# Kernel tuning notes

Hardware: AMD Instinct MI355X
Metric: run time of the kernel (lower is better)

Reference implementation:

```python
import jax, jax.numpy as jnp
import numpy as np

B, N, E, D, L, NC = 48, 96, 1024, 300, 4, 7
NEG = 1e30


def _gru(x, h, w_ih, w_hh, b_ih, b_hh):
    # torch.nn.GRUCell math; weights are (3D, D) in torch layout
    gi = x @ w_ih.T + b_ih
    gh = h @ w_hh.T + b_hh
    ir, iz, inn = jnp.split(gi, 3, axis=-1)
    hr, hz, hn = jnp.split(gh, 3, axis=-1)
    r = jax.nn.sigmoid(ir + hr)
    z = jax.nn.sigmoid(iz + hz)
    n = jnp.tanh(inn + r * hn)
    return (1.0 - z) * n + z * h


def _layer(Cin, Hin, adj, cwi, cwh, cbi, cbh, pwi, pwh, pbi, pbh, wq, wk, gb):
    b, n, d = Cin.shape
    zeros = jnp.zeros((b, d), Cin.dtype)
    c0 = _gru(Cin[:, 0], zeros, cwi, cwh, cbi, cbh)          # GRUCell with h=0
    p0 = _gru(zeros, Cin[:, 0], pwi, pwh, pbi, pbh)          # M=0 at step 0
    P0 = jnp.zeros_like(Cin).at[:, 0].set(p0)                # growing P kept as full buffer
    pos = jnp.arange(n)

    def step(P, i):
        q = Cin[:, i]                                        # (B, D)
        mask = adj[:, i] * (pos < i).astype(adj.dtype)       # only predecessors j < i
        # GatLinear: Linear(cat(Q,K)) == Q.wq + K.wk + b
        alpha = (q @ wq)[:, None] + P @ wk + gb              # (B, N)
        alpha = alpha - (1.0 - mask) * NEG                   # mask_logic
        w = jax.nn.softmax(alpha, axis=-1)
        M = jnp.einsum('bn,bnd->bd', w, P)
        c_i = _gru(q, M, cwi, cwh, cbi, cbh)
        p_i = _gru(M, Hin[:, i], pwi, pwh, pbi, pbh)
        P = jax.lax.dynamic_update_slice(P, p_i[:, None, :], (0, i, 0))
        return P, c_i

    P, Cs = jax.lax.scan(step, P0, jnp.arange(1, n))
    CL = jnp.concatenate([c0[:, None], jnp.moveaxis(Cs, 0, 1)], axis=1)  # (B, N, D)
    return CL, P


def reference(features, adj, s_mask, fc1_w, fc1_b,
              gc_wih, gc_whh, gc_bih, gc_bhh,
              gp_wih, gp_whh, gp_bih, gp_bhh,
              gat_wq, gat_wk, gat_b,
              mlp_w0, mlp_b0, mlp_w1, mlp_b1, mlp_w2, mlp_b2):
    # s_mask is unused when no_rel_attn=True (faithful to torch forward)
    H0 = jax.nn.relu(features @ fc1_w + fc1_b)
    H_list = [H0]
    C_list = [H0]
    for l in range(L):
        CL, P = _layer(C_list[l], H_list[l], adj,
                       gc_wih[l], gc_whh[l], gc_bih[l], gc_bhh[l],
                       gp_wih[l], gp_whh[l], gp_bih[l], gp_bhh[l],
                       gat_wq[l], gat_wk[l], gat_b[l])
        C_list.append(CL)
        H_list.append(CL)
        H_list.append(P)
    H_list.append(features)
    H = jnp.concatenate(H_list, axis=2)                      # (B, N, 9D + E)
    x = jax.nn.relu(H @ mlp_w0 + mlp_b0)
    x = jax.nn.relu(x @ mlp_w1 + mlp_b1)
    logits = x @ mlp_w2 + mlp_b2                             # (B, N, NC)
    return logits


def setup_inputs() -> dict:
    key = jax.random.key(0)
    ks = jax.random.split(key, 25)
    s = 0.02

    def p(k, shape):
        return jax.random.normal(k, shape, jnp.float32) * s

    features = jax.random.normal(ks[0], (B, N, E), jnp.float32)
    # DAG adjacency: random predecessors, strictly lower-triangular, previous
    # utterance always connected (guarantees a nonempty attention context)
    base = jax.random.bernoulli(ks[1], 0.5, (B, N, N)).astype(jnp.float32)
    tri = jnp.tril(jnp.ones((N, N), jnp.float32), -1)
    prev = jnp.eye(N, k=-1, dtype=jnp.float32)
    adj = jnp.maximum(base * tri, prev[None])
    s_mask = jax.random.randint(ks[2], (B, N, N), 0, 2, jnp.int32)
    in_dim = D * (2 * L + 1) + E
    return {
        'features': features, 'adj': adj, 's_mask': s_mask,
        'fc1_w': p(ks[3], (E, D)), 'fc1_b': p(ks[4], (D,)),
        'gc_wih': p(ks[5], (L, 3 * D, D)), 'gc_whh': p(ks[6], (L, 3 * D, D)),
        'gc_bih': p(ks[7], (L, 3 * D)), 'gc_bhh': p(ks[8], (L, 3 * D)),
        'gp_wih': p(ks[9], (L, 3 * D, D)), 'gp_whh': p(ks[10], (L, 3 * D, D)),
        'gp_bih': p(ks[11], (L, 3 * D)), 'gp_bhh': p(ks[12], (L, 3 * D)),
        'gat_wq': p(ks[13], (L, D)), 'gat_wk': p(ks[14], (L, D)), 'gat_b': p(ks[15], (L,)),
        'mlp_w0': p(ks[16], (in_dim, D)), 'mlp_b0': p(ks[17], (D,)),
        'mlp_w1': p(ks[18], (D, D)), 'mlp_b1': p(ks[19], (D,)),
        'mlp_w2': p(ks[20], (D, NC)), 'mlp_b2': p(ks[21], (NC,)),
    }
```

## Files before the change

### kernel.cpp

```cpp
#include <hip/hip_runtime.h>
#include <math.h>

#define BB 48
#define NN 96
#define EE 1024
#define DD 300
#define LL 4
#define G3 900
#define PP 150
#define PP2 152
#define NC4 38
#define HDIM 3724
#define ROWS (BB*NN)
#define NEGI -1.0e30f
#define KP300 304
#define GIC_TILES 540

#define NLDS 6
#define NPIN 14

typedef _Float16 half2_t __attribute__((ext_vector_type(2)));
typedef _Float16 h8 __attribute__((ext_vector_type(8)));
typedef float f4 __attribute__((ext_vector_type(4)));

__device__ __forceinline__ float sigm(float x){
    return __fdividef(1.0f, 1.0f + __expf(-x));
}
__device__ __forceinline__ float ftanh(float x){
    float e = __expf(2.0f*x);
    return 1.0f - __fdividef(2.0f, e + 1.0f);
}

__device__ __forceinline__ void dot4(const h8 wv, const h8 mc,
                                     float& a0, float& a1, float& a2, float& a3)
{
    half2_t w0,w1,w2,w3,m0,m1,m2,m3;
    w0.x=wv[0]; w0.y=wv[1]; m0.x=mc[0]; m0.y=mc[1];
    w1.x=wv[2]; w1.y=wv[3]; m1.x=mc[2]; m1.y=mc[3];
    w2.x=wv[4]; w2.y=wv[5]; m2.x=mc[4]; m2.y=mc[5];
    w3.x=wv[6]; w3.y=wv[7]; m3.x=mc[6]; m3.y=mc[7];
    a0 = __builtin_amdgcn_fdot2(w0, m0, a0, false);
    a1 = __builtin_amdgcn_fdot2(w1, m1, a1, false);
    a2 = __builtin_amdgcn_fdot2(w2, m2, a2, false);
    a3 = __builtin_amdgcn_fdot2(w3, m3, a3, false);
}

__global__ __launch_bounds__(256) void pack_w_q(const float* __restrict__ src_all,
                                                h8* __restrict__ dst)
{
    int l = blockIdx.y;
    int idx = blockIdx.x*256 + threadIdx.x;
    if (idx >= NC4*G3) return;
    int c = idx / G3, gate = idx % G3;
    const float* src = src_all + (size_t)l*G3*DD + (size_t)gate*DD;
    h8 v;
    #pragma unroll
    for (int j=0;j<8;j++){
        int d = 8*c + j;
        v[j] = (d<DD) ? (_Float16)src[d] : (_Float16)0.f;
    }
    dst[(size_t)l*NC4*G3 + idx] = v;
}

__global__ __launch_bounds__(256) void conv_gru_w(const float* __restrict__ gp_whh,
                                                  const float* __restrict__ gc_wih,
                                                  const float* __restrict__ gc_whh,
                                                  _Float16* __restrict__ outp)
{
    int z = blockIdx.y; int l = z/3, wsel = z%3;
    const float* src = (wsel==0?gp_whh:wsel==1?gc_wih:gc_whh) + (size_t)l*G3*DD;
    _Float16* dst = outp + (size_t)z*G3*KP300;
    int idx = blockIdx.x*256 + threadIdx.x;
    if (idx >= G3*KP300) return;
    int n = idx/KP300, k = idx%KP300;
    dst[idx] = (k<DD) ? (_Float16)src[(size_t)n*DD+k] : (_Float16)0.f;
}

__global__ __launch_bounds__(256) void convT(const float* __restrict__ src,
                                             _Float16* __restrict__ dst,
                                             int K, int N, int Kpad)
{
    int idx = blockIdx.x*256 + threadIdx.x;
    if (idx >= N*Kpad) return;
    int n = idx/Kpad, k = idx%Kpad;
    dst[idx] = (k<K) ? (_Float16)src[(size_t)k*N + n] : (_Float16)0.f;
}

__device__ __forceinline__ void gemm_tile(
    int m0, int n0, int tid,
    const float* __restrict__ A, int lda,
    const _Float16* __restrict__ B, int Kpad,
    const float* __restrict__ bias,
    float* __restrict__ C, int ldc,
    int N, int K, int relu,
    _Float16 (*As)[40], _Float16 (*Bs)[40])
{
    int w = tid>>6, lane = tid&63;
    int wy = w>>1, wx = w&1;
    int lm = lane&15, q = lane>>4;

    f4 acc[4][2];
    #pragma unroll
    for (int a=0;a<4;a++)
        #pragma unroll
        for (int b=0;b<2;b++)
            #pragma unroll
            for (int r=0;r<4;r++) acc[a][b][r]=0.f;

    int am = tid>>1, akg = (tid&1)*16;
    int bn = tid>>2, bkg = (tid&3)*8;
    const float* arow = A + (size_t)(m0+am)*lda;

    for (int k0=0; k0<K; k0+=32){
        {
            __align__(16) _Float16 av[16];
            #pragma unroll
            for (int u=0;u<16;u+=4){
                int k = k0 + akg + u;
                float x0,x1,x2,x3;
                if (k+4 <= K){
                    float4 v = *(const float4*)(arow + k);
                    x0=v.x;x1=v.y;x2=v.z;x3=v.w;
                } else {
                    x0 = (k  <K)? arow[k  ]:0.f;
                    x1 = (k+1<K)? arow[k+1]:0.f;
                    x2 = (k+2<K)? arow[k+2]:0.f;
                    x3 = (k+3<K)? arow[k+3]:0.f;
                }
                av[u]=(_Float16)x0; av[u+1]=(_Float16)x1;
                av[u+2]=(_Float16)x2; av[u+3]=(_Float16)x3;
            }
            *(h8*)&As[am][akg]   = *(h8*)&av[0];
            *(h8*)&As[am][akg+8] = *(h8*)&av[8];
        }
        {
            int gk = k0 + bkg;
            h8 bv;
            #pragma unroll
            for (int j=0;j<8;j++) bv[j]=(_Float16)0.f;
            if (n0+bn < N && gk < Kpad)
                bv = *(const h8*)(B + (size_t)(n0+bn)*Kpad + gk);
            *(h8*)&Bs[bn][bkg] = bv;
        }
        __syncthreads();
        h8 af[4], bf[2];
        #pragma unroll
        for (int mb=0; mb<4; mb++) af[mb] = *(h8*)&As[wy*64+mb*16+lm][q*8];
        #pragma unroll
        for (int nb=0; nb<2; nb++) bf[nb] = *(h8*)&Bs[wx*32+nb*16+lm][q*8];
        #pragma unroll
        for (int mb=0; mb<4; mb++)
            #pragma unroll
            for (int nb=0; nb<2; nb++)
                acc[mb][nb] = __builtin_amdgcn_mfma_f32_16x16x32_f16(af[mb], bf[nb], acc[mb][nb], 0,0,0);
        __syncthreads();
    }
    #pragma unroll
    for (int mb=0; mb<4; mb++){
        int r0 = m0 + wy*64 + mb*16 + q*4;
        #pragma unroll
        for (int nb=0; nb<2; nb++){
            int c = n0 + wx*32 + nb*16 + lm;
            if (c < N){
                float bb = bias[c];
                #pragma unroll
                for (int reg=0; reg<4; reg++){
                    float v = acc[mb][nb][reg] + bb;
                    if (relu) v = fmaxf(v, 0.f);
                    C[(size_t)(r0+reg)*ldc + c] = v;
                }
            }
        }
    }
}

__global__ __launch_bounds__(256) void gemm_mfma(
    const float* __restrict__ A, int lda,
    const _Float16* __restrict__ B, int Kpad,
    const float* __restrict__ bias,
    float* __restrict__ C, int ldc,
    int N, int K, int relu)
{
    __shared__ _Float16 As[128][40];
    __shared__ _Float16 Bs[64][40];
    gemm_tile(blockIdx.y*128, blockIdx.x*64, threadIdx.x,
              A, lda, B, Kpad, bias, C, ldc, N, K, relu, As, Bs);
}

__global__ void featcopy(const float* __restrict__ f, float* __restrict__ H)
{
    size_t row = blockIdx.x;
    int t = threadIdx.x;
    float4 v = *(const float4*)(f + row*EE + t*4);
    *(float4*)(H + row*HDIM + 2700 + t*4) = v;
}

__global__ void __launch_bounds__(1024)
__attribute__((amdgpu_waves_per_eu(4,4)))
scan_kernel(
    float* __restrict__ Hbuf,
    const float* __restrict__ GHp,
    const h8* __restrict__ pwiQ,
    const h8* __restrict__ pwhQ,
    const float* __restrict__ pbi,
    const float* __restrict__ pbh,
    const float* __restrict__ wk,
    const float* __restrict__ wq,
    const float* __restrict__ gat_b, int lidx,
    const float* __restrict__ adj,
    float* __restrict__ Mbuf,
    int ccol, int hcol, int pcol,
    const _Float16* __restrict__ cwiF,
    const float* __restrict__ cbi,
    float* __restrict__ GIc)
{
    __shared__ __align__(16) char pool[158976];
    (void)wq; (void)gat_b; (void)lidx;

    if (blockIdx.x >= BB){
        if (threadIdx.x < 256){
            _Float16 (*As)[40] = (_Float16 (*)[40])pool;
            _Float16 (*Bs)[40] = (_Float16 (*)[40])(pool + 128*40*2);
            int bid = blockIdx.x - BB;
            int n0 = (bid % 15)*64, m0 = (bid / 15)*128;
            gemm_tile(m0, n0, threadIdx.x, Hbuf + ccol, HDIM, cwiF, KP300,
                      cbi, GIc, G3, G3, DD, 0, As, Bs);
        }
        return;
    }

    int b = blockIdx.x;
    int t = threadIdx.x;

    half2_t (*P_h2)[PP]   = (half2_t (*)[PP])(pool);
    h8*      Wlds         = (h8*)(pool + 57600);
    float*   g_s          = (float*)(pool + 144000);
    float  (*Mpart)[DD]   = (float (*)[DD])(pool + 147600);
    float*   ghp_s        = (float*)(pool + 151200);
    float*   hv_s         = (float*)(pool + 154800);
    half2_t* M_h2         = (half2_t*)(pool + 156000);
    float*   e_s          = (float*)(pool + 156640);
    float*   pk_s         = (float*)(pool + 157024);
    float*   pksum        = (float*)(pool + 157408);
    unsigned (*adjb)[4]   = (unsigned (*)[4])(pool + 157440);

    size_t rowbase = (size_t)b*NN;

    float pbi_r = (t < G3) ? pbi[t] : 0.f;
    float2 wk_r = make_float2(0.f,0.f);
    if (t < PP) wk_r = *(const float2*)&wk[2*t];

    h8 wp0,wp1,wp2,wp3,wp4,wp5,wp6,wp7,wp8,wp9,wp10,wp11,wp12,wp13;
    if (t < G3){
        const h8* W = pwiQ + t;
        wp0 = W[(size_t)6*G3];   wp1 = W[(size_t)7*G3];   wp2 = W[(size_t)8*G3];
        wp3 = W[(size_t)9*G3];   wp4 = W[(size_t)10*G3];  wp5 = W[(size_t)11*G3];
        wp6 = W[(size_t)12*G3];  wp7 = W[(size_t)13*G3];  wp8 = W[(size_t)14*G3];
        wp9 = W[(size_t)15*G3];  wp10 = W[(size_t)16*G3]; wp11 = W[(size_t)17*G3];
        wp12 = W[(size_t)18*G3]; wp13 = W[(size_t)19*G3];
        asm volatile("" : "+v"(wp0),"+v"(wp1),"+v"(wp2),"+v"(wp3),
                          "+v"(wp4),"+v"(wp5),"+v"(wp6));
        asm volatile("" : "+v"(wp7),"+v"(wp8),"+v"(wp9),"+v"(wp10),
                          "+v"(wp11),"+v"(wp12),"+v"(wp13));
    }

    for (int idx=t; idx<NLDS*G3; idx+=1024)
        Wlds[idx] = pwiQ[idx];
    if (t < NN*3){
        int r = t/3, w = t%3;
        const float* arow = adj + (rowbase + r)*NN + w*32;
        unsigned m = 0;
        for (int c=0;c<32;c++) if (arow[c] != 0.f) m |= (1u<<c);
        adjb[r][w] = m;
    }
    if (t < PP){
        float2 c2 = *(const float2*)&Hbuf[rowbase*HDIM + ccol + 2*t];
        Mpart[0][2*t] = c2.x; Mpart[0][2*t+1] = c2.y;
        half2_t mh; mh.x = (_Float16)c2.x; mh.y = (_Float16)c2.y;
        M_h2[t] = mh;
    } else if (t < PP2){
        half2_t z; z.x=(_Float16)0.f; z.y=(_Float16)0.f;
        M_h2[t] = z;
    }
    __syncthreads();
    if (t < G3){
        const h8* W2 = pwhQ + t;
        float a0=0.f, a1=0.f, a2=0.f, a3=0.f;
        #pragma unroll 4
        for (int c=0;c<NC4;c++){
            h8 wv = W2[(size_t)c*G3];
            h8 mc = *(h8*)&M_h2[4*c];
            dot4(wv, mc, a0,a1,a2,a3);
        }
        g_s[t] = pbh[t] + (a0+a2) + (a1+a3);
    }
    __syncthreads();
    if (t < 192){
        float pw = 0.f;
        if (t < PP){
            int d0 = 2*t, d1 = 2*t+1;
            float r0  = sigm(pbi[d0]      + g_s[d0]);
            float z0  = sigm(pbi[DD+d0]   + g_s[DD+d0]);
            float n0  = ftanh(pbi[2*DD+d0] + r0*g_s[2*DD+d0]);
            float p0  = (1.f-z0)*n0 + z0*Mpart[0][d0];
            float r1  = sigm(pbi[d1]      + g_s[d1]);
            float z1  = sigm(pbi[DD+d1]   + g_s[DD+d1]);
            float n1  = ftanh(pbi[2*DD+d1] + r1*g_s[2*DD+d1]);
            float p1  = (1.f-z1)*n1 + z1*Mpart[0][d1];
            *(float2*)&Hbuf[rowbase*HDIM + pcol + d0] = make_float2(p0,p1);
            half2_t ph; ph.x = (_Float16)p0; ph.y = (_Float16)p1;
            P_h2[0][t] = ph;
            pw = p0*wk_r.x + p1*wk_r.y;
            *(float2*)&Mbuf[rowbase*DD + d0] = make_float2(0.f,0.f);
        }
        #pragma unroll
        for (int o=32;o>0;o>>=1) pw += __shfl_xor(pw,o);
        if ((t&63)==0) pksum[t>>6] = pw;
    }
    __syncthreads();

    float m_run = NEGI;

    for (int i=1;i<NN;i++){
        size_t row = rowbase + i;
        if (t < 64){
            float s_last = pksum[0]+pksum[1]+pksum[2];
            if (t==0) pk_s[i-1] = s_last;
            m_run = fmaxf(m_run, s_last);
            float a0 = NEGI, a1 = NEGI;
            if (t < i){
                if ((adjb[i][t>>5]>>(t&31))&1u) a0 = (t==i-1)? s_last : pk_s[t];
            }
            int j1 = 64+t;
            if (t < 32 && j1 < i){
                if ((adjb[i][2]>>t)&1u) a1 = (j1==i-1)? s_last : pk_s[j1];
            }
            float e0 = __expf(a0 - m_run);
            float e1 = (t<32)? __expf(a1 - m_run) : 0.f;
            float ss = e0+e1;
            #pragma unroll
            for (int o=32;o>0;o>>=1) ss += __shfl_xor(ss,o);
            float inv = __fdividef(1.f, ss);
            e_s[t] = e0*inv;
            if (t<32) e_s[64+t] = e1*inv;
        }
        __syncthreads();
        if (t < 450){
            int g = t/150, dp = t%150;
            int cnt = (i+2)/3;
            int j0 = g*cnt; int j1 = j0+cnt; if (j1 > i) j1 = i;
            float m0=0.f, m1=0.f;
            #pragma unroll 4
            for (int j=j0;j<j1;j++){
                float w = e_s[j];
                half2_t pv = P_h2[j][dp];
                m0 += w*(float)pv.x;
                m1 += w*(float)pv.y;
            }
            *(float2*)&Mpart[g][2*dp] = make_float2(m0,m1);
        } else if (t >= 512){
            int k = t-512;
            #pragma unroll
            for (int it=0; it<2; it++){
                int idx = k + it*512;
                if (idx < 450){
                    *(float2*)&ghp_s[2*idx] = *(const float2*)&GHp[row*G3 + 2*idx];
                } else if (idx < 600){
                    int h = idx-450;
                    *(float2*)&hv_s[2*h] = *(const float2*)&Hbuf[row*HDIM + hcol + 2*h];
                }
            }
        }
        __syncthreads();
        if (t < PP){
            float m0 = Mpart[0][2*t] + Mpart[1][2*t] + Mpart[2][2*t];
            float m1 = Mpart[0][2*t+1] + Mpart[1][2*t+1] + Mpart[2][2*t+1];
            half2_t mh; mh.x = (_Float16)m0; mh.y = (_Float16)m1;
            M_h2[t] = mh;
            *(float2*)&Mbuf[row*DD + 2*t] = make_float2(m0,m1);
        }
        __syncthreads();
        if (t < G3){
            const h8* W = pwiQ + t;
            const h8* Mc = (const h8*)M_h2;
            float a0=0.f, a1=0.f, a2=0.f, a3=0.f;
            dot4(Wlds[t],        Mc[0], a0,a1,a2,a3);
            dot4(Wlds[G3+t],     Mc[1], a0,a1,a2,a3);
            dot4(Wlds[2*G3+t],   Mc[2], a0,a1,a2,a3);
            dot4(Wlds[3*G3+t],   Mc[3], a0,a1,a2,a3);
            dot4(Wlds[4*G3+t],   Mc[4], a0,a1,a2,a3);
            dot4(Wlds[5*G3+t],   Mc[5], a0,a1,a2,a3);
            dot4(wp0,  Mc[6],  a0,a1,a2,a3);
            dot4(wp1,  Mc[7],  a0,a1,a2,a3);
            dot4(wp2,  Mc[8],  a0,a1,a2,a3);
            dot4(wp3,  Mc[9],  a0,a1,a2,a3);
            dot4(wp4,  Mc[10], a0,a1,a2,a3);
            dot4(wp5,  Mc[11], a0,a1,a2,a3);
            dot4(wp6,  Mc[12], a0,a1,a2,a3);
            dot4(wp7,  Mc[13], a0,a1,a2,a3);
            dot4(wp8,  Mc[14], a0,a1,a2,a3);
            dot4(wp9,  Mc[15], a0,a1,a2,a3);
            dot4(wp10, Mc[16], a0,a1,a2,a3);
            dot4(wp11, Mc[17], a0,a1,a2,a3);
            dot4(wp12, Mc[18], a0,a1,a2,a3);
            dot4(wp13, Mc[19], a0,a1,a2,a3);
            #pragma unroll 6
            for (int c=NLDS+NPIN;c<NC4;c++){
                h8 wv = W[(size_t)c*G3];
                dot4(wv, Mc[c], a0,a1,a2,a3);
            }
            g_s[t] = pbi_r + (a0+a2) + (a1+a3);
        }
        __syncthreads();
        if (t < 192){
            float pw = 0.f;
            if (t < PP){
                int d0 = 2*t, d1 = 2*t+1;
                float2 hv = *(const float2*)&hv_s[d0];
                float r0  = sigm(g_s[d0]      + ghp_s[d0]);
                float z0  = sigm(g_s[DD+d0]   + ghp_s[DD+d0]);
                float n0  = ftanh(g_s[2*DD+d0] + r0*ghp_s[2*DD+d0]);
                float p0  = (1.f-z0)*n0 + z0*hv.x;
                float r1  = sigm(g_s[d1]      + ghp_s[d1]);
                float z1  = sigm(g_s[DD+d1]   + ghp_s[DD+d1]);
                float n1  = ftanh(g_s[2*DD+d1] + r1*ghp_s[2*DD+d1]);
                float p1  = (1.f-z1)*n1 + z1*hv.y;
                *(float2*)&Hbuf[row*HDIM + pcol + d0] = make_float2(p0,p1);
                half2_t ph; ph.x = (_Float16)p0; ph.y = (_Float16)p1;
                P_h2[i][t] = ph;
                pw = p0*wk_r.x + p1*wk_r.y;
            }
            #pragma unroll
            for (int o=32;o>0;o>>=1) pw += __shfl_xor(pw,o);
            if ((t&63)==0) pksum[t>>6] = pw;
        }
        __syncthreads();
    }
}

__global__ __launch_bounds__(320) void combine_c(
    const float* __restrict__ GIc, const float* __restrict__ GHc,
    const float* __restrict__ Mbuf, float* __restrict__ Hbuf, int clcol)
{
    size_t row = blockIdx.x;
    int d = threadIdx.x;
    if (d < DD){
        float ir = GIc[row*G3+d], iz = GIc[row*G3+DD+d], inn = GIc[row*G3+2*DD+d];
        float hr = GHc[row*G3+d], hz = GHc[row*G3+DD+d], hn  = GHc[row*G3+2*DD+d];
        float r  = sigm(ir+hr);
        float z  = sigm(iz+hz);
        float nn = ftanh(inn + r*hn);
        float h  = Mbuf[row*DD+d];
        Hbuf[row*HDIM + clcol + d] = (1.f-z)*nn + z*h;
    }
}

__global__ __launch_bounds__(64) void logits_kernel(
    const float* __restrict__ x2, const float* __restrict__ w2,
    const float* __restrict__ b2, float* __restrict__ out)
{
    size_t row = blockIdx.x;
    int lane = threadIdx.x;
    float acc[7]={0,0,0,0,0,0,0};
    for (int d=lane; d<DD; d+=64){
        float x = x2[row*DD+d];
        #pragma unroll
        for (int c=0;c<7;c++) acc[c] += x*w2[d*7+c];
    }
    #pragma unroll
    for (int c=0;c<7;c++){
        float s = acc[c];
        #pragma unroll
        for (int o=32;o>0;o>>=1) s += __shfl_down(s,o);
        if (lane==0) out[row*7+c] = s + b2[c];
    }
}

extern "C" void kernel_launch(void* const* d_in, const int* in_sizes, int n_in,
                              void* d_out, int out_size, void* d_ws, size_t ws_size,
                              hipStream_t stream)
{
    const float* features = (const float*)d_in[0];
    const float* adj      = (const float*)d_in[1];
    const float* fc1_w    = (const float*)d_in[3];
    const float* fc1_b    = (const float*)d_in[4];
    const float* gc_wih   = (const float*)d_in[5];
    const float* gc_whh   = (const float*)d_in[6];
    const float* gc_bih   = (const float*)d_in[7];
    const float* gc_bhh   = (const float*)d_in[8];
    const float* gp_wih   = (const float*)d_in[9];
    const float* gp_whh   = (const float*)d_in[10];
    const float* gp_bih   = (const float*)d_in[11];
    const float* gp_bhh   = (const float*)d_in[12];
    const float* gat_wq   = (const float*)d_in[13];
    const float* gat_wk   = (const float*)d_in[14];
    const float* gat_b    = (const float*)d_in[15];
    const float* mlp_w0   = (const float*)d_in[16];
    const float* mlp_b0   = (const float*)d_in[17];
    const float* mlp_w1   = (const float*)d_in[18];
    const float* mlp_b1   = (const float*)d_in[19];
    const float* mlp_w2   = (const float*)d_in[20];
    const float* mlp_b2   = (const float*)d_in[21];
    float* out = (float*)d_out;

    float* ws = (float*)d_ws;
    size_t off = 0;
    float* Hbuf = ws + off; off += (size_t)ROWS*HDIM;
    float* bufA = ws + off; off += (size_t)ROWS*G3;
    float* bufB = ws + off; off += (size_t)ROWS*G3;
    float* bufC = ws + off; off += (size_t)ROWS*G3;
    float* Mbuf = ws + off; off += (size_t)ROWS*DD;
    h8* pwiQ = (h8*)(ws + off); off += (size_t)LL*NC4*G3*4;
    h8* pwhQ = (h8*)(ws + off); off += (size_t)LL*NC4*G3*4;
    _Float16* gruF = (_Float16*)(ws + off); off += (size_t)12*G3*KP300/2;
    _Float16* fc1F = (_Float16*)(ws + off); off += (size_t)DD*EE/2;
    _Float16* mlp0F= (_Float16*)(ws + off); off += (size_t)DD*3728/2;
    _Float16* mlp1F= (_Float16*)(ws + off); off += (size_t)DD*KP300/2;
    (void)ws_size; (void)in_sizes; (void)n_in; (void)out_size;

    {
        pack_w_q<<<dim3((NC4*G3+255)/256, LL), 256, 0, stream>>>(gp_wih, pwiQ);
        pack_w_q<<<dim3((NC4*G3+255)/256, LL), 256, 0, stream>>>(gp_whh, pwhQ);
        conv_gru_w<<<dim3((G3*KP300+255)/256, 12), 256, 0, stream>>>(gp_whh, gc_wih, gc_whh, gruF);
        convT<<<(DD*EE+255)/256, 256, 0, stream>>>(fc1_w, fc1F, EE, DD, EE);
        convT<<<(DD*3728+255)/256, 256, 0, stream>>>(mlp_w0, mlp0F, HDIM, DD, 3728);
        convT<<<(DD*KP300+255)/256, 256, 0, stream>>>(mlp_w1, mlp1F, DD, DD, KP300);
    }
    gemm_mfma<<<dim3(5,36),256,0,stream>>>(features, EE, fc1F, EE, fc1_b,
                                           Hbuf, HDIM, DD, EE, 1);
    featcopy<<<ROWS,256,0,stream>>>(features, Hbuf);

    for (int l=0;l<LL;l++){
        int ccol  = (l==0)? 0 : 300 + (l-1)*600;
        int hcol  = l*300;
        int pcol  = 600 + l*600;
        int clcol = 300 + l*600;
        const h8* pwiQl = pwiQ + (size_t)l*NC4*G3;
        const h8* pwhQl = pwhQ + (size_t)l*NC4*G3;
        const _Float16* pwhF = gruF + (size_t)(l*3+0)*G3*KP300;
        const _Float16* cwiF = gruF + (size_t)(l*3+1)*G3*KP300;
        const _Float16* cwhF = gruF + (size_t)(l*3+2)*G3*KP300;

        gemm_mfma<<<dim3(15,36),256,0,stream>>>(Hbuf+hcol, HDIM, pwhF, KP300,
                                                gp_bhh + l*G3, bufA, G3, G3, DD, 0);
        scan_kernel<<<BB+GIC_TILES,1024,0,stream>>>(Hbuf, bufA, pwiQl, pwhQl,
                                          gp_bih + l*G3, gp_bhh + l*G3,
                                          gat_wk + l*DD, gat_wq + l*DD, gat_b, l,
                                          adj, Mbuf, ccol, hcol, pcol,
                                          cwiF, gc_bih + l*G3, bufB);
        gemm_mfma<<<dim3(15,36),256,0,stream>>>(Mbuf, DD, cwhF, KP300,
                                                gc_bhh + l*G3, bufC, G3, G3, DD, 0);
        combine_c<<<ROWS,320,0,stream>>>(bufB, bufC, Mbuf, Hbuf, clcol);
    }

    gemm_mfma<<<dim3(5,36),256,0,stream>>>(Hbuf, HDIM, mlp0F, 3728, mlp_b0,
                                           bufB, DD, DD, HDIM, 1);
    gemm_mfma<<<dim3(5,36),256,0,stream>>>(bufB, DD, mlp1F, KP300, mlp_b1,
                                           bufC, DD, DD, DD, 1);
    logits_kernel<<<ROWS,64,0,stream>>>(bufC, mlp_w2, mlp_b2, out);
}
```

Baseline: 2.676 ms.

## Compact active attention edges via ballot and split weighted sum four ways

The softmax stage now uses wave ballots and popcounts to write a compacted list of (index, weight) pairs for only the adjacency-active predecessors. The weighted P reduction then iterates over that list only, skipping masked entries that previously contributed zero. The reduction is split across four thread groups instead of three. The GHp/H prefetch is reassigned to a separate thread range and uses float4 loads. Shared memory grows slightly to hold the pair list and an extra partial-sum row, and the gathered P row indices make the access pattern less regular.

New measurement: 2.622 ms. 2.0% less time.

```diff
diff --git a/kernel.cpp b/kernel.cpp
--- a/kernel.cpp
+++ b/kernel.cpp
@@ -214,7 +214,7 @@
     const float* __restrict__ cbi,
     float* __restrict__ GIc)
 {
-    __shared__ __align__(16) char pool[158976];
+    __shared__ __align__(16) char pool[160576];
     (void)wq; (void)gat_b; (void)lidx;
 
     if (blockIdx.x >= BB){
@@ -236,13 +236,14 @@
     h8*      Wlds         = (h8*)(pool + 57600);
     float*   g_s          = (float*)(pool + 144000);
     float  (*Mpart)[DD]   = (float (*)[DD])(pool + 147600);
-    float*   ghp_s        = (float*)(pool + 151200);
-    float*   hv_s         = (float*)(pool + 154800);
-    half2_t* M_h2         = (half2_t*)(pool + 156000);
-    float*   e_s          = (float*)(pool + 156640);
-    float*   pk_s         = (float*)(pool + 157024);
-    float*   pksum        = (float*)(pool + 157408);
-    unsigned (*adjb)[4]   = (unsigned (*)[4])(pool + 157440);
+    float*   ghp_s        = (float*)(pool + 152400);
+    float*   hv_s         = (float*)(pool + 156000);
+    half2_t* M_h2         = (half2_t*)(pool + 157200);
+    float*   pk_s         = (float*)(pool + 157840);
+    float*   pksum        = (float*)(pool + 158224);
+    float2*  cpair        = (float2*)(pool + 158256);
+    int*     ncnt_s       = (int*)(pool + 159024);
+    unsigned (*adjb)[4]   = (unsigned (*)[4])(pool + 159040);
 
     size_t rowbase = (size_t)b*NN;
 
@@ -327,54 +328,66 @@
             float s_last = pksum[0]+pksum[1]+pksum[2];
             if (t==0) pk_s[i-1] = s_last;
             m_run = fmaxf(m_run, s_last);
+            bool act0 = false, act1 = false;
             float a0 = NEGI, a1 = NEGI;
-            if (t < i){
-                if ((adjb[i][t>>5]>>(t&31))&1u) a0 = (t==i-1)? s_last : pk_s[t];
+            if (t < i && ((adjb[i][t>>5]>>(t&31))&1u)){
+                act0 = true;
+                a0 = (t==i-1)? s_last : pk_s[t];
             }
             int j1 = 64+t;
-            if (t < 32 && j1 < i){
-                if ((adjb[i][2]>>t)&1u) a1 = (j1==i-1)? s_last : pk_s[j1];
-            }
-            float e0 = __expf(a0 - m_run);
-            float e1 = (t<32)? __expf(a1 - m_run) : 0.f;
+            if (t < 32 && j1 < i && ((adjb[i][2]>>t)&1u)){
+                act1 = true;
+                a1 = (j1==i-1)? s_last : pk_s[j1];
+            }
+            float e0 = act0 ? __expf(a0 - m_run) : 0.f;
+            float e1 = act1 ? __expf(a1 - m_run) : 0.f;
             float ss = e0+e1;
             #pragma unroll
             for (int o=32;o>0;o>>=1) ss += __shfl_xor(ss,o);
             float inv = __fdividef(1.f, ss);
-            e_s[t] = e0*inv;
-            if (t<32) e_s[64+t] = e1*inv;
-        }
-        __syncthreads();
-        if (t < 450){
+            unsigned long long mask0 = __ballot(act0);
+            unsigned long long mask1 = __ballot(act1);
+            unsigned long long lt = (1ull<<t)-1ull;
+            int base = __popcll(mask0);
+            if (act0){
+                int pos0 = __popcll(mask0 & lt);
+                cpair[pos0] = make_float2(__int_as_float(t), e0*inv);
+            }
+            if (act1){
+                int pos1 = base + __popcll(mask1 & lt);
+                cpair[pos1] = make_float2(__int_as_float(j1), e1*inv);
+            }
+            if (t==0) ncnt_s[0] = base + __popcll(mask1);
+        }
+        __syncthreads();
+        if (t < 600){
+            int nact = ncnt_s[0];
             int g = t/150, dp = t%150;
-            int cnt = (i+2)/3;
-            int j0 = g*cnt; int j1 = j0+cnt; if (j1 > i) j1 = i;
+            int cnt = (nact+3)>>2;
+            int j0 = g*cnt; int jend = j0+cnt; if (jend > nact) jend = nact;
             float m0=0.f, m1=0.f;
             #pragma unroll 4
-            for (int j=j0;j<j1;j++){
-                float w = e_s[j];
+            for (int jj=j0;jj<jend;jj++){
+                float2 pr = cpair[jj];
+                int j = __float_as_int(pr.x);
                 half2_t pv = P_h2[j][dp];
-                m0 += w*(float)pv.x;
-                m1 += w*(float)pv.y;
+                m0 += pr.y*(float)pv.x;
+                m1 += pr.y*(float)pv.y;
             }
             *(float2*)&Mpart[g][2*dp] = make_float2(m0,m1);
-        } else if (t >= 512){
-            int k = t-512;
-            #pragma unroll
-            for (int it=0; it<2; it++){
-                int idx = k + it*512;
-                if (idx < 450){
-                    *(float2*)&ghp_s[2*idx] = *(const float2*)&GHp[row*G3 + 2*idx];
-                } else if (idx < 600){
-                    int h = idx-450;
-                    *(float2*)&hv_s[2*h] = *(const float2*)&Hbuf[row*HDIM + hcol + 2*h];
-                }
+        } else if (t >= 640 && t < 940){
+            int idx = t-640;
+            if (idx < 225)
+                *(float4*)&ghp_s[idx*4] = *(const float4*)&GHp[row*G3 + idx*4];
+            else {
+                int h = idx-225;
+                *(float4*)&hv_s[h*4] = *(const float4*)&Hbuf[row*HDIM + hcol + h*4];
             }
         }
         __syncthreads();
         if (t < PP){
-            float m0 = Mpart[0][2*t] + Mpart[1][2*t] + Mpart[2][2*t];
-            float m1 = Mpart[0][2*t+1] + Mpart[1][2*t+1] + Mpart[2][2*t+1];
+            float m0 = Mpart[0][2*t]+Mpart[1][2*t]+Mpart[2][2*t]+Mpart[3][2*t];
+            float m1 = Mpart[0][2*t+1]+Mpart[1][2*t+1]+Mpart[2][2*t+1]+Mpart[3][2*t+1];
             half2_t mh; mh.x = (_Float16)m0; mh.y = (_Float16)m1;
             M_h2[t] = mh;
             *(float2*)&Mbuf[row*DD + 2*t] = make_float2(m0,m1);
```
